# Optimization experiments

Hardware: AMD Instinct MI355X
Metric: run time of the kernel (lower is better)

The kernel has to match this reference:

```python
import jax, jax.numpy as jnp
import numpy as np

D_MODEL = 1024
N_HEADS = 16
D_HEAD = D_MODEL // N_HEADS
GN_EPS = 1e-5


def setup_inputs() -> dict:
    key = jax.random.key(0)
    ks = jax.random.split(key, 5)
    B, T = 2, 2048
    s = 1.0 / np.sqrt(D_MODEL)
    x = jax.random.normal(ks[0], (B, T, D_MODEL), dtype=jnp.float32)
    W_q = jax.random.normal(ks[1], (D_MODEL, D_MODEL), dtype=jnp.float32) * s
    W_k = jax.random.normal(ks[2], (D_MODEL, D_MODEL), dtype=jnp.float32) * s
    W_v = jax.random.normal(ks[3], (D_MODEL, D_MODEL), dtype=jnp.float32) * s
    W_o = jax.random.normal(ks[4], (D_MODEL, D_MODEL), dtype=jnp.float32) * s
    gn_weight = jnp.ones((D_MODEL,), dtype=jnp.float32)
    gn_bias = jnp.zeros((D_MODEL,), dtype=jnp.float32)
    return {"x": x, "W_q": W_q, "W_k": W_k, "W_v": W_v, "W_o": W_o,
            "gn_weight": gn_weight, "gn_bias": gn_bias}


def reference(x, W_q, W_k, W_v, W_o, gn_weight, gn_bias):
    B, T, _ = x.shape
    H, Dh = N_HEADS, D_HEAD
    # Projections (nn.Linear: y = x @ W.T), split heads -> [B, T, H, Dh]
    q = (x @ W_q.T).reshape(B, T, H, Dh)
    k = (x @ W_k.T).reshape(B, T, H, Dh)
    v = (x @ W_v.T).reshape(B, T, H, Dh)

    # Per-head causal decay mask D_h[i, j] = gamma_h^(i-j) for i >= j else 0
    gammas = jnp.asarray([1.0 - 2.0 ** (-5.0 - i) for i in range(H)],
                         dtype=jnp.float32)  # [H]
    idx = jnp.arange(T, dtype=jnp.float32)
    diff = idx[:, None] - idx[None, :]  # [T, T]
    decay = jnp.where(diff >= 0,
                      gammas[:, None, None] ** jnp.maximum(diff, 0.0),
                      0.0)  # [H, T, T]

    scale = jnp.sqrt(jnp.asarray(Dh, dtype=x.dtype))
    qk = jnp.einsum('bthd,bshd->bhts', q, k)          # [B, H, T, T]
    attn = qk * decay[None] / scale
    y = jnp.einsum('bhts,bshd->bthd', attn, v)        # [B, T, H, Dh]

    # GroupNorm(n_heads groups) over channels-last-transposed layout:
    # torch applies it to [B, d_model, T]; each group = one head's Dh channels,
    # normalized over (Dh, T).
    yg = y.transpose(0, 2, 3, 1)                      # [B, H, Dh, T]
    mean = yg.mean(axis=(2, 3), keepdims=True)
    var = yg.var(axis=(2, 3), keepdims=True)
    yn = (yg - mean) / jnp.sqrt(var + GN_EPS)
    yn = yn * gn_weight.reshape(1, H, Dh, 1) + gn_bias.reshape(1, H, Dh, 1)
    y = yn.transpose(0, 3, 1, 2).reshape(B, T, H * Dh)  # [B, T, d_model]
    return y @ W_o.T
```

## Files before the change

### kernel.cpp

```cpp
#include <hip/hip_runtime.h>
#include <math.h>

#define TSEQ 2048
#define NB   2
#define DM   1024
#define NH   16
#define DH   64
#define GN_EPS 1e-5f

typedef short v8s __attribute__((ext_vector_type(8)));
typedef short v4s __attribute__((ext_vector_type(4)));
typedef float v4f __attribute__((ext_vector_type(4)));

__device__ __forceinline__ short f2bf(float f) {
    union { float f; unsigned u; } c; c.f = f;
    unsigned u = c.u;
    unsigned r = (u + 0x7fffu + ((u >> 16) & 1u)) >> 16;
    return (short)r;
}
__device__ __forceinline__ float bf2f(short s) {
    union { unsigned u; float f; } c; c.u = ((unsigned)(unsigned short)s) << 16;
    return c.f;
}

__device__ __forceinline__ unsigned cvtpk_bf16(float lo, float hi) {
    unsigned r;
    asm("v_cvt_pk_bf16_f32 %0, %1, %2" : "=v"(r) : "v"(lo), "v"(hi));
    return r;
}

__device__ __forceinline__ void gl_lds16(const void* g, void* l) {
    __builtin_amdgcn_global_load_lds(
        (const __attribute__((address_space(1))) void*)g,
        (__attribute__((address_space(3))) void*)l, 16, 0, 0);
}

__global__ __launch_bounds__(256) void cast_kernel(
    const float* __restrict__ x,
    const float* __restrict__ Wq, const float* __restrict__ Wk,
    const float* __restrict__ Wv, const float* __restrict__ Wo,
    short* __restrict__ xbf, short* __restrict__ wbf)
{
    const int NX = NB * TSEQ * DM;
    const int NW = DM * DM;
    const int total4 = (NX + 4 * NW) / 4;
    for (int i = blockIdx.x * 256 + threadIdx.x; i < total4;
         i += gridDim.x * 256) {
        int e = i * 4;
        const float* src; short* dst;
        if (e < NX) { src = x + e; dst = xbf + e; }
        else {
            int o = e - NX;
            int w = o >> 20;
            int r = o & (NW - 1);
            src = (w == 0 ? Wq : w == 1 ? Wk : w == 2 ? Wv : Wo) + r;
            dst = wbf + o;
        }
        v4f v = *(const v4f*)src;
        v4s s;
        #pragma unroll
        for (int j = 0; j < 4; ++j) s[j] = f2bf(v[j]);
        *(v4s*)dst = s;
    }
}

template <bool SWAP>
__device__ __forceinline__ void mm_loop(
    const char* Agp, const char* Bgp, short* Asm, short* Bsm,
    int t, int lr, int g, int wr, int wc, v4f acc[4][4])
{
    int soff[4], sdst[4];
    #pragma unroll
    for (int p = 0; p < 4; ++p) {
        int i = p * 256 + t;
        int row = i >> 3;
        int cp  = (i & 7) * 16;
        soff[p] = row * (DM * 2) + (cp ^ ((row & 7) << 4));
        sdst[p] = (p * 256 + (t & 192)) * 16;
    }
    const int swz = (lr & 7) << 4;

    for (int kt = 0; kt < DM / 64; ++kt) {
        const int kb = kt * 128;
        #pragma unroll
        for (int p = 0; p < 4; ++p) {
            gl_lds16(Agp + (size_t)soff[p] + kb, (char*)Asm + sdst[p]);
            gl_lds16(Bgp + (size_t)soff[p] + kb, (char*)Bsm + sdst[p]);
        }
        asm volatile("s_waitcnt vmcnt(0)" ::: "memory");
        __syncthreads();

        v8s bfr[4][2];
        #pragma unroll
        for (int j = 0; j < 4; ++j) {
            int rowb = wc + j * 16 + lr;
            #pragma unroll
            for (int ks = 0; ks < 2; ++ks)
                bfr[j][ks] = *(const v8s*)((const char*)Bsm + rowb * 128
                               + ((ks * 64 + g * 16) ^ swz));
        }
        #pragma unroll
        for (int i = 0; i < 4; ++i) {
            int rowa = wr + i * 16 + lr;
            v8s a0 = *(const v8s*)((const char*)Asm + rowa * 128 + ((g * 16) ^ swz));
            v8s a1 = *(const v8s*)((const char*)Asm + rowa * 128 + ((64 + g * 16) ^ swz));
            #pragma unroll
            for (int j = 0; j < 4; ++j) {
                if (SWAP) {
                    acc[i][j] = __builtin_amdgcn_mfma_f32_16x16x32_bf16(
                        bfr[j][0], a0, acc[i][j], 0, 0, 0);
                    acc[i][j] = __builtin_amdgcn_mfma_f32_16x16x32_bf16(
                        bfr[j][1], a1, acc[i][j], 0, 0, 0);
                } else {
                    acc[i][j] = __builtin_amdgcn_mfma_f32_16x16x32_bf16(
                        a0, bfr[j][0], acc[i][j], 0, 0, 0);
                    acc[i][j] = __builtin_amdgcn_mfma_f32_16x16x32_bf16(
                        a1, bfr[j][1], acc[i][j], 0, 0, 0);
                }
            }
        }
        __syncthreads();
    }
}

__global__ __launch_bounds__(256, 3) void gemm_qkv_mfma(
    const short* __restrict__ xbf, const short* __restrict__ wbf,
    short* __restrict__ Qb, short* __restrict__ Kb,
    short* __restrict__ Kt, short* __restrict__ Vt)
{
    const int bid = blockIdx.x;
    const int swizb = (bid & 7) * 96 + (bid >> 3);
    const int z = swizb >> 8;
    const int rem = swizb & 255;
    const int n0 = (rem & 7) * 128, m0 = (rem >> 3) * 128;

    const int t = threadIdx.x, l = t & 63, w = t >> 6;
    const int wr = (w >> 1) * 64, wc = (w & 1) * 64;
    const int lr = l & 15, g = l >> 4, lg4 = g * 4;

    __shared__ short As[128 * 64];
    __shared__ short Bs[128 * 64];

    v4f acc[4][4];
    #pragma unroll
    for (int i = 0; i < 4; ++i)
        #pragma unroll
        for (int j = 0; j < 4; ++j) acc[i][j] = (v4f){0.f, 0.f, 0.f, 0.f};

    const char* Agp = (const char*)(xbf + (size_t)m0 * DM);
    const char* Bgp = (const char*)(wbf + (size_t)z * (DM * DM) + (size_t)n0 * DM);

    if (z == 0) {
        mm_loop<true>(Agp, Bgp, As, Bs, t, lr, g, wr, wc, acc);
        const int head = (n0 + wc) >> 6;
        const float l2g = log2f(1.0f - exp2f(-5.0f - (float)head));
        float fac[4];
        #pragma unroll
        for (int i = 0; i < 4; ++i) {
            int tl = (m0 + wr + i * 16 + lr) & 63;
            fac[i] = exp2f(fmaf(l2g, (float)tl, -3.0f));
        }
        #pragma unroll
        for (int i = 0; i < 4; ++i) {
            int mrow = m0 + wr + i * 16 + lr;
            #pragma unroll
            for (int j = 0; j < 4; ++j) {
                int ncol = n0 + wc + j * 16 + lg4;
                v4s pk;
                #pragma unroll
                for (int r = 0; r < 4; ++r) pk[r] = f2bf(acc[i][j][r] * fac[i]);
                *(v4s*)(Qb + (size_t)mrow * DM + ncol) = pk;
            }
        }
    } else if (z == 1) {
        mm_loop<false>(Agp, Bgp, As, Bs, t, lr, g, wr, wc, acc);
        float l2gj[4];
        #pragma unroll
        for (int j = 0; j < 4; ++j) {
            int hh = (n0 + wc + j * 16 + lr) >> 6;
            l2gj[j] = -log2f(1.0f - exp2f(-5.0f - (float)hh));
        }
        #pragma unroll
        for (int i = 0; i < 4; ++i) {
            int row  = m0 + wr + i * 16 + lg4;
            int bidx = row >> 11, tb = row & (TSEQ - 1);
            #pragma unroll
            for (int j = 0; j < 4; ++j) {
                int col = n0 + wc + j * 16 + lr;
                v4s pk;
                #pragma unroll
                for (int r = 0; r < 4; ++r) {
                    int tl = (row + r) & 63;
                    float fc = exp2f(l2gj[j] * (float)tl);
                    short bv = f2bf(acc[i][j][r] * fc);
                    Kb[(size_t)(row + r) * DM + col] = bv;
                    pk[r] = bv;
                }
                *(v4s*)(Kt + ((size_t)bidx << 21) + ((size_t)col << 11) + tb) = pk;
            }
        }
    } else {
        mm_loop<false>(Agp, Bgp, As, Bs, t, lr, g, wr, wc, acc);
        #pragma unroll
        for (int i = 0; i < 4; ++i) {
            int row  = m0 + wr + i * 16 + lg4;
            int bidx = row >> 11, tb = row & (TSEQ - 1);
            #pragma unroll
            for (int j = 0; j < 4; ++j) {
                int col = n0 + wc + j * 16 + lr;
                v4s pk;
                #pragma unroll
                for (int r = 0; r < 4; ++r) pk[r] = f2bf(acc[i][j][r]);
                *(v4s*)(Vt + ((size_t)bidx << 21) + ((size_t)col << 11) + tb) = pk;
            }
        }
    }
}

__global__ __launch_bounds__(256, 2) void chunk_kv(
    const short* __restrict__ Kt, const short* __restrict__ Vt,
    short* __restrict__ At)
{
    const int bid = blockIdx.x;
    const int c = bid & 31, bh = bid >> 5;
    const int b = bh >> 4, h = bh & 15;
    const int tid = threadIdx.x, l = tid & 63, w = tid >> 6;
    const int lr = l & 15, g = l >> 4;

    const size_t rowbase = ((size_t)b * DM + h * 64);

    v8s kf[2], vf[4][2];
    {
        const short* kp = Kt + (rowbase + 16 * w + lr) * TSEQ + 64 * c;
        kf[0] = *(const v8s*)(kp + g * 8);
        kf[1] = *(const v8s*)(kp + 32 + g * 8);
    }
    #pragma unroll
    for (int j = 0; j < 4; ++j) {
        const short* vp = Vt + (rowbase + j * 16 + lr) * TSEQ + 64 * c;
        vf[j][0] = *(const v8s*)(vp + g * 8);
        vf[j][1] = *(const v8s*)(vp + 32 + g * 8);
    }

    v4f acc[4];
    #pragma unroll
    for (int j = 0; j < 4; ++j) acc[j] = (v4f){0.f, 0.f, 0.f, 0.f};

    #pragma unroll
    for (int j = 0; j < 4; ++j) {
        acc[j] = __builtin_amdgcn_mfma_f32_16x16x32_bf16(kf[0], vf[j][0], acc[j], 0, 0, 0);
        acc[j] = __builtin_amdgcn_mfma_f32_16x16x32_bf16(kf[1], vf[j][1], acc[j], 0, 0, 0);
    }

    short* Ab = At + (((size_t)bh * 32 + c) << 12);
    #pragma unroll
    for (int j = 0; j < 4; ++j) {
        v4s pk;
        #pragma unroll
        for (int r = 0; r < 4; ++r) pk[r] = f2bf(acc[j][r]);
        *(v4s*)(Ab + (j * 16 + lr) * 64 + 16 * w + g * 4) = pk;
    }
}

__global__ __launch_bounds__(256) void chunk_scan(
    const short* __restrict__ At, short* __restrict__ St)
{
    const int idx = blockIdx.x * 256 + threadIdx.x;
    const int bh = idx >> 12;
    const int h  = bh & 15;
    const float l2g = log2f(1.0f - exp2f(-5.0f - (float)h));
    const float g64 = exp2f(l2g * 64.0f);

    const size_t base = ((size_t)bh << 17) + (idx & 4095);
    float state = 0.0f;
    #pragma unroll
    for (int c = 1; c < 32; ++c) {
        float a = bf2f(At[base + ((size_t)(c - 1) << 12)]);
        state = g64 * (state + a);
        St[base + ((size_t)c << 12)] = f2bf(state);
    }
}

__global__ __launch_bounds__(256, 2) void chunk_out(
    const short* __restrict__ Qb, const short* __restrict__ Kb,
    const short* __restrict__ Vt, const short* __restrict__ St,
    short* __restrict__ Ybf, float* __restrict__ psums)
{
    const int bid = blockIdx.x;
    const int xcd = bid & 7, r8 = bid >> 3;
    const int bh  = xcd * 4 + (r8 >> 5);
    const int c   = r8 & 31;
    const int b = bh >> 4, h = bh & 15;
    const int tid = threadIdx.x, l = tid & 63, w = tid >> 6;
    const int lr = l & 15, g = l >> 4;

    __shared__ short strip[64 * 64];
    __shared__ float tr[64][68];
    __shared__ float red[8];

    const size_t rowQK = ((size_t)(b * TSEQ + 64 * c)) * DM + h * 64;

    v8s qf[4][2];
    #pragma unroll
    for (int j = 0; j < 4; ++j) {
        const short* qp = Qb + rowQK + (size_t)(j * 16 + lr) * DM;
        qf[j][0] = *(const v8s*)(qp + g * 8);
        qf[j][1] = *(const v8s*)(qp + 32 + g * 8);
    }
    v8s kf0, kf1;
    {
        const short* kp = Kb + rowQK + (size_t)(16 * w + lr) * DM;
        kf0 = *(const v8s*)(kp + g * 8);
        kf1 = *(const v8s*)(kp + 32 + g * 8);
    }
    v8s sf0 = {}, sf1 = {};
    if (c > 0) {
        const short* sp = St + (((size_t)bh * 32 + c) << 12) + (16 * w + lr) * 64;
        sf0 = *(const v8s*)(sp + g * 8);
        sf1 = *(const v8s*)(sp + 32 + g * 8);
    }
    v8s vf0, vf1;
    {
        const short* vp = Vt + ((size_t)(b * DM + h * 64) + 16 * w + lr) * TSEQ
                          + 64 * c;
        vf0 = *(const v8s*)(vp + g * 8);
        vf1 = *(const v8s*)(vp + 32 + g * 8);
    }

    v4f s[4];
    #pragma unroll
    for (int j = 0; j < 4; ++j) {
        v4f a = (v4f){0.f, 0.f, 0.f, 0.f};
        a = __builtin_amdgcn_mfma_f32_16x16x32_bf16(kf0, qf[j][0], a, 0, 0, 0);
        a = __builtin_amdgcn_mfma_f32_16x16x32_bf16(kf1, qf[j][1], a, 0, 0, 0);
        s[j] = a;
    }

    v4f y[4];
    #pragma unroll
    for (int j = 0; j < 4; ++j) y[j] = (v4f){0.f, 0.f, 0.f, 0.f};
    if (c > 0) {
        #pragma unroll
        for (int j = 0; j < 4; ++j) {
            y[j] = __builtin_amdgcn_mfma_f32_16x16x32_bf16(sf0, qf[j][0], y[j], 0, 0, 0);
            y[j] = __builtin_amdgcn_mfma_f32_16x16x32_bf16(sf1, qf[j][1], y[j], 0, 0, 0);
        }
    }

    #pragma unroll
    for (int j = 0; j < 4; ++j) {
        v4f vv = s[j];
        #pragma unroll
        for (int r = 0; r < 4; ++r)
            if ((j * 16 + lr) - (16 * w + g * 4 + r) < 0) vv[r] = 0.0f;
        unsigned u0 = cvtpk_bf16(vv[0], vv[1]);
        unsigned u1 = cvtpk_bf16(vv[2], vv[3]);
        int byte = ((j * 16 + lr) * 128 + 32 * w + g * 8) ^ ((lr & 7) << 4);
        *(unsigned long long*)((char*)strip + byte) =
            (unsigned long long)u0 | ((unsigned long long)u1 << 32);
    }
    __syncthreads();

    #pragma unroll
    for (int j = 0; j < 4; ++j) {
        int rb = (j * 16 + lr) * 128;
        int sw = (lr & 7) << 4;
        v8s sB0 = *(const v8s*)((char*)strip + ((rb + g * 16) ^ sw));
        v8s sB1 = *(const v8s*)((char*)strip + ((rb + 64 + g * 16) ^ sw));
        y[j] = __builtin_amdgcn_mfma_f32_16x16x32_bf16(vf0, sB0, y[j], 0, 0, 0);
        y[j] = __builtin_amdgcn_mfma_f32_16x16x32_bf16(vf1, sB1, y[j], 0, 0, 0);
    }

    float lsum = 0.f, lsq = 0.f;
    #pragma unroll
    for (int j = 0; j < 4; ++j)
        #pragma unroll
        for (int r = 0; r < 4; ++r) {
            float vy = y[j][r];
            lsum += vy; lsq += vy * vy;
        }
    #pragma unroll
    for (int m = 32; m; m >>= 1) {
        lsum += __shfl_xor(lsum, m, 64);
        lsq  += __shfl_xor(lsq,  m, 64);
    }
    if (l == 0) { red[w] = lsum; red[4 + w] = lsq; }

    #pragma unroll
    for (int j = 0; j < 4; ++j)
        #pragma unroll
        for (int r = 0; r < 4; ++r)
            tr[j * 16 + lr][16 * w + g * 4 + r] = y[j][r];
    __syncthreads();

    if (tid == 0) {
        float* ps = psums + ((size_t)bh * 32 + c) * 2;
        ps[0] = red[0] + red[1] + red[2] + red[3];
        ps[1] = red[4] + red[5] + red[6] + red[7];
    }

    #pragma unroll
    for (int u = 0; u < 4; ++u) {
        int row  = (tid >> 4) + u * 16;
        int col4 = (tid & 15) * 4;
        v4f val = *(const v4f*)&tr[row][col4];
        v4s pk;
        #pragma unroll
        for (int r = 0; r < 4; ++r) pk[r] = f2bf(val[r]);
        *(v4s*)&Ybf[(size_t)(b * TSEQ + 64 * c + row) * DM + h * 64 + col4] = pk;
    }
}

__global__ __launch_bounds__(256) void gn_finalize(
    const float* __restrict__ psums,
    const float* __restrict__ gnw, const float* __restrict__ gnb,
    float* __restrict__ scale, float* __restrict__ shift)
{
    int idx = blockIdx.x * 256 + threadIdx.x;
    if (idx >= NB * DM) return;
    int bb = idx >> 10;
    int ch = idx & (DM - 1);
    int hh = ch >> 6;
    int bh = bb * 16 + hh;

    float s = 0.f, q = 0.f;
    #pragma unroll
    for (int k = 0; k < 32; ++k) {
        s += psums[((size_t)bh * 32 + k) * 2];
        q += psums[((size_t)bh * 32 + k) * 2 + 1];
    }
    const float n = (float)(DH * TSEQ);
    float mean = s / n;
    float var  = q / n - mean * mean;
    float rstd = rsqrtf(var + GN_EPS);
    float sc = rstd * gnw[ch];
    scale[idx] = sc;
    shift[idx] = gnb[ch] - mean * sc;
}

__global__ __launch_bounds__(256) void wo_prep(
    const short* __restrict__ Wob, const float* __restrict__ scale,
    const float* __restrict__ shift,
    short* __restrict__ Wo2, float* __restrict__ bias)
{
    const int tid = threadIdx.x, l = tid & 63, w = tid >> 6;
    const int bn = blockIdx.x * 4 + w;
    const int b = bn >> 10, n = bn & 1023;
    const int k0 = l * 16;

    const short* wp = Wob + (size_t)n * DM + k0;
    v8s w0 = *(const v8s*)wp;
    v8s w1 = *(const v8s*)(wp + 8);
    const float* sc = scale + b * DM + k0;
    const float* sh = shift + b * DM + k0;

    v8s o0, o1;
    float bsum = 0.f;
    #pragma unroll
    for (int j = 0; j < 8; ++j) {
        float wf = bf2f(w0[j]);
        o0[j] = f2bf(wf * sc[j]);
        bsum = fmaf(sh[j], wf, bsum);
    }
    #pragma unroll
    for (int j = 0; j < 8; ++j) {
        float wf = bf2f(w1[j]);
        o1[j] = f2bf(wf * sc[8 + j]);
        bsum = fmaf(sh[8 + j], wf, bsum);
    }
    short* op = Wo2 + ((size_t)b * DM + n) * DM + k0;
    *(v8s*)op = o0;
    *(v8s*)(op + 8) = o1;

    #pragma unroll
    for (int m = 32; m; m >>= 1) bsum += __shfl_xor(bsum, m, 64);
    if (l == 0) bias[bn] = bsum;
}

__global__ __launch_bounds__(256, 3) void gemm_out_mfma(
    const short* __restrict__ Ybf, const short* __restrict__ Wo2,
    const float* __restrict__ bias, float* __restrict__ out)
{
    const int bid = blockIdx.x;
    const int swizb = (bid & 7) * 32 + (bid >> 3);
    const int n0 = (swizb & 7) * 128, m0 = (swizb >> 3) * 128;
    const int b = m0 >> 11;
    const int t = threadIdx.x, l = t & 63, w = t >> 6;
    const int wr = (w >> 1) * 64, wc = (w & 1) * 64;
    const int lr = l & 15, g = l >> 4;

    __shared__ short As[128 * 64];
    __shared__ short Bs[128 * 64];

    v4f acc[4][4];
    #pragma unroll
    for (int i = 0; i < 4; ++i)
        #pragma unroll
        for (int j = 0; j < 4; ++j) acc[i][j] = (v4f){0.f, 0.f, 0.f, 0.f};

    const char* Agp = (const char*)(Ybf + (size_t)m0 * DM);
    const char* Bgp = (const char*)(Wo2 + (size_t)b * DM * DM + (size_t)n0 * DM);

    mm_loop<true>(Agp, Bgp, As, Bs, t, lr, g, wr, wc, acc);

    #pragma unroll
    for (int i = 0; i < 4; ++i) {
        int mrow = m0 + wr + i * 16 + lr;
        #pragma unroll
        for (int j = 0; j < 4; ++j) {
            int ncol = n0 + wc + j * 16 + g * 4;
            v4f bv = *(const v4f*)&bias[b * DM + ncol];
            v4f o = acc[i][j] + bv;
            *(v4f*)&out[(size_t)mrow * DM + ncol] = o;
        }
    }
}

extern "C" void kernel_launch(void* const* d_in, const int* in_sizes, int n_in,
                              void* d_out, int out_size, void* d_ws, size_t ws_size,
                              hipStream_t stream)
{
    const float* x   = (const float*)d_in[0];
    const float* Wq  = (const float*)d_in[1];
    const float* Wk  = (const float*)d_in[2];
    const float* Wv  = (const float*)d_in[3];
    const float* Wo  = (const float*)d_in[4];
    const float* gnw = (const float*)d_in[5];
    const float* gnb = (const float*)d_in[6];
    float* out = (float*)d_out;

    char* wsb = (char*)d_ws;
    size_t o = 0;
    short* Qb   = (short*)(wsb + o); o += (size_t)NB * TSEQ * DM * 2;
    short* Kb   = (short*)(wsb + o); o += (size_t)NB * TSEQ * DM * 2;
    short* Kt   = (short*)(wsb + o); o += (size_t)NB * TSEQ * DM * 2;
    short* Vt   = (short*)(wsb + o); o += (size_t)NB * TSEQ * DM * 2;
    short* xbf  = (short*)(wsb + o); o += (size_t)NB * TSEQ * DM * 2;
    short* wbf  = (short*)(wsb + o); o += (size_t)4 * DM * DM * 2;
    short* Ybf  = (short*)(wsb + o); o += (size_t)NB * TSEQ * DM * 2;
    short* St   = (short*)(wsb + o); o += (size_t)NB * TSEQ * DM * 2;
    short* Wo2  = (short*)(wsb + o); o += (size_t)NB * DM * DM * 2;
    float* psums = (float*)(wsb + o); o += (size_t)32 * 32 * 2 * 4;
    float* scale = (float*)(wsb + o); o += (size_t)NB * DM * 4;
    float* shift = (float*)(wsb + o); o += (size_t)NB * DM * 4;
    float* bias  = (float*)(wsb + o); o += (size_t)NB * DM * 4;
    if (ws_size < o) return;

    short* At = xbf;

    cast_kernel<<<2048, 256, 0, stream>>>(x, Wq, Wk, Wv, Wo, xbf, wbf);
    gemm_qkv_mfma<<<dim3(768), 256, 0, stream>>>(xbf, wbf, Qb, Kb, Kt, Vt);
    chunk_kv<<<dim3(1024), 256, 0, stream>>>(Kt, Vt, At);
    chunk_scan<<<dim3(512), 256, 0, stream>>>(At, St);
    chunk_out<<<dim3(1024), 256, 0, stream>>>(Qb, Kb, Vt, St, Ybf, psums);
    gn_finalize<<<dim3((NB * DM + 255) / 256), 256, 0, stream>>>(
        psums, gnw, gnb, scale, shift);
    wo_prep<<<dim3(512), 256, 0, stream>>>(
        wbf + 3 * (size_t)DM * DM, scale, shift, Wo2, bias);
    gemm_out_mfma<<<dim3(256), 256, 0, stream>>>(Ybf, Wo2, bias, out);
}
```

Measured before the change: 94.03 us.

## Double-buffer LDS tiles in GEMM main loop to overlap loads with MFMA

```diff
diff --git a/kernel.cpp b/kernel.cpp
--- a/kernel.cpp
+++ b/kernel.cpp
@@ -65,8 +65,8 @@
 }
 
 template <bool SWAP>
-__device__ __forceinline__ void mm_loop(
-    const char* Agp, const char* Bgp, short* Asm, short* Bsm,
+__device__ __forceinline__ void mm_loop_db(
+    const char* Agp, const char* Bgp, char* lds,
     int t, int lr, int g, int wr, int wc, v4f acc[4][4])
 {
     int soff[4], sdst[4];
@@ -80,15 +80,26 @@
     }
     const int swz = (lr & 7) << 4;
 
+    #pragma unroll
+    for (int p = 0; p < 4; ++p) {
+        gl_lds16(Agp + (size_t)soff[p], lds + sdst[p]);
+        gl_lds16(Bgp + (size_t)soff[p], lds + 16384 + sdst[p]);
+    }
+
     for (int kt = 0; kt < DM / 64; ++kt) {
-        const int kb = kt * 128;
-        #pragma unroll
-        for (int p = 0; p < 4; ++p) {
-            gl_lds16(Agp + (size_t)soff[p] + kb, (char*)Asm + sdst[p]);
-            gl_lds16(Bgp + (size_t)soff[p] + kb, (char*)Bsm + sdst[p]);
-        }
+        const char* cur = lds + (kt & 1) * 32768;
         asm volatile("s_waitcnt vmcnt(0)" ::: "memory");
         __syncthreads();
+
+        if (kt < DM / 64 - 1) {
+            char* nxt = lds + ((kt + 1) & 1) * 32768;
+            const int kb = (kt + 1) * 128;
+            #pragma unroll
+            for (int p = 0; p < 4; ++p) {
+                gl_lds16(Agp + (size_t)soff[p] + kb, nxt + sdst[p]);
+                gl_lds16(Bgp + (size_t)soff[p] + kb, nxt + 16384 + sdst[p]);
+            }
+        }
 
         v8s bfr[4][2];
         #pragma unroll
@@ -96,14 +107,14 @@
             int rowb = wc + j * 16 + lr;
             #pragma unroll
             for (int ks = 0; ks < 2; ++ks)
-                bfr[j][ks] = *(const v8s*)((const char*)Bsm + rowb * 128
+                bfr[j][ks] = *(const v8s*)(cur + 16384 + rowb * 128
                                + ((ks * 64 + g * 16) ^ swz));
         }
         #pragma unroll
         for (int i = 0; i < 4; ++i) {
             int rowa = wr + i * 16 + lr;
-            v8s a0 = *(const v8s*)((const char*)Asm + rowa * 128 + ((g * 16) ^ swz));
-            v8s a1 = *(const v8s*)((const char*)Asm + rowa * 128 + ((64 + g * 16) ^ swz));
+            v8s a0 = *(const v8s*)(cur + rowa * 128 + ((g * 16) ^ swz));
+            v8s a1 = *(const v8s*)(cur + rowa * 128 + ((64 + g * 16) ^ swz));
             #pragma unroll
             for (int j = 0; j < 4; ++j) {
                 if (SWAP) {
@@ -119,11 +130,10 @@
                 }
             }
         }
-        __syncthreads();
-    }
-}
-
-__global__ __launch_bounds__(256, 3) void gemm_qkv_mfma(
+    }
+}
+
+__global__ __launch_bounds__(256, 2) void gemm_qkv_mfma(
     const short* __restrict__ xbf, const short* __restrict__ wbf,
     short* __restrict__ Qb, short* __restrict__ Kb,
     short* __restrict__ Kt, short* __restrict__ Vt)
@@ -138,8 +148,7 @@
     const int wr = (w >> 1) * 64, wc = (w & 1) * 64;
     const int lr = l & 15, g = l >> 4, lg4 = g * 4;
 
-    __shared__ short As[128 * 64];
-    __shared__ short Bs[128 * 64];
+    __shared__ char lds[65536];
 
     v4f acc[4][4];
     #pragma unroll
@@ -151,7 +160,7 @@
     const char* Bgp = (const char*)(wbf + (size_t)z * (DM * DM) + (size_t)n0 * DM);
 
     if (z == 0) {
-        mm_loop<true>(Agp, Bgp, As, Bs, t, lr, g, wr, wc, acc);
+        mm_loop_db<true>(Agp, Bgp, lds, t, lr, g, wr, wc, acc);
         const int head = (n0 + wc) >> 6;
         const float l2g = log2f(1.0f - exp2f(-5.0f - (float)head));
         float fac[4];
@@ -173,7 +182,7 @@
             }
         }
     } else if (z == 1) {
-        mm_loop<false>(Agp, Bgp, As, Bs, t, lr, g, wr, wc, acc);
+        mm_loop_db<false>(Agp, Bgp, lds, t, lr, g, wr, wc, acc);
         float l2gj[4];
         #pragma unroll
         for (int j = 0; j < 4; ++j) {
@@ -200,7 +209,7 @@
             }
         }
     } else {
-        mm_loop<false>(Agp, Bgp, As, Bs, t, lr, g, wr, wc, acc);
+        mm_loop_db<false>(Agp, Bgp, lds, t, lr, g, wr, wc, acc);
         #pragma unroll
         for (int i = 0; i < 4; ++i) {
             int row  = m0 + wr + i * 16 + lg4;
@@ -477,7 +486,7 @@
     if (l == 0) bias[bn] = bsum;
 }
 
-__global__ __launch_bounds__(256, 3) void gemm_out_mfma(
+__global__ __launch_bounds__(256, 2) void gemm_out_mfma(
     const short* __restrict__ Ybf, const short* __restrict__ Wo2,
     const float* __restrict__ bias, float* __restrict__ out)
 {
@@ -489,8 +498,7 @@
     const int wr = (w >> 1) * 64, wc = (w & 1) * 64;
     const int lr = l & 15, g = l >> 4;
 
-    __shared__ short As[128 * 64];
-    __shared__ short Bs[128 * 64];
+    __shared__ char lds[65536];
 
     v4f acc[4][4];
     #pragma unroll
@@ -501,7 +509,7 @@
     const char* Agp = (const char*)(Ybf + (size_t)m0 * DM);
     const char* Bgp = (const char*)(Wo2 + (size_t)b * DM * DM + (size_t)n0 * DM);
 
-    mm_loop<true>(Agp, Bgp, As, Bs, t, lr, g, wr, wc, acc);
+    mm_loop_db<true>(Agp, Bgp, lds, t, lr, g, wr, wc, acc);
 
     #pragma unroll
     for (int i = 0; i < 4; ++i) {
```

New measurement: 89.78 us. -4.5%, faster.
